# Optimization experiments

Hardware: AMD Instinct MI355X
Metric: run time of the kernel (lower is better)

Reference implementation:

```python
import jax, jax.numpy as jnp
import numpy as np

BLOCK_SIZE = 64
TOP_K = 4
D_MODEL = 256


def setup_inputs() -> dict:
    key = jax.random.key(0)
    kq, kk, kv = jax.random.split(key, 3)
    B, N, D = 4, 4096, D_MODEL
    q = jax.random.normal(kq, (B, N, D), dtype=jnp.float32)
    k = jax.random.normal(kk, (B, N, D), dtype=jnp.float32)
    v = jax.random.normal(kv, (B, N, D), dtype=jnp.float32)
    return {"q": q, "k": k, "v": v}


def _block_sparse_mask(q, k):
    # q, k: (B, N, D). Returns (B, N, N) bool mask (True = keep).
    B, N, D = q.shape
    nb = N // BLOCK_SIZE
    q_cent = q.reshape(B, nb, BLOCK_SIZE, D).mean(axis=2)  # (B, nb, D)
    k_cent = k.reshape(B, nb, BLOCK_SIZE, D).mean(axis=2)  # (B, nb, D)
    # pairwise Euclidean distance between centroids (nb is small: 64)
    diff = q_cent[:, :, None, :] - k_cent[:, None, :, :]   # (B, nb, nb, D)
    dist = jnp.sqrt(jnp.sum(diff * diff, axis=-1))          # (B, nb, nb)
    kk_ = min(TOP_K, nb)
    _, top_idx = jax.lax.top_k(-dist, kk_)                  # smallest distances
    mask = jnp.zeros((B, nb, nb), dtype=bool)
    b_idx = jnp.arange(B)[:, None, None]
    r_idx = jnp.arange(nb)[None, :, None]
    mask = mask.at[b_idx, r_idx, top_idx].set(True)
    # expand block mask to full (B, N, N) via broadcast-reshape
    mask_full = jnp.broadcast_to(
        mask[:, :, None, :, None], (B, nb, BLOCK_SIZE, nb, BLOCK_SIZE)
    ).reshape(B, N, N)
    return mask_full


def reference(q, k, v):
    mask = _block_sparse_mask(q, k)
    scale = 1.0 / (D_MODEL ** 0.5)
    scores = jnp.einsum('bqd,bkd->bqk', q, k) * scale       # (B, N, N)
    scores = jnp.where(mask, scores, -jnp.inf)
    attn = jax.nn.softmax(scores, axis=-1)
    out = jnp.einsum('bqk,bkd->bqd', attn, v)               # (B, N, D)
    return out
```

## Files before the change

kernel.cpp:

```cpp
#include <hip/hip_runtime.h>
#include <math.h>
#include <stdint.h>

#define BATCH 4
#define NSEQ 4096
#define DM 256
#define BLK 64
#define NB 64
#define TOPK 4

typedef unsigned short u16;
typedef unsigned int u32;
typedef __attribute__((ext_vector_type(8))) short bf16x8;
typedef __attribute__((ext_vector_type(4))) float f32x4;

__device__ __forceinline__ u16 f2bf(float f) {
    union { float f; u32 u; } c{f};
    u32 r = c.u + 0x7FFFu + ((c.u >> 16) & 1u);
    return (u16)(r >> 16);
}
__device__ __forceinline__ float bf2f(u16 h) {
    union { u32 u; float f; } c{((u32)h) << 16};
    return c.f;
}

__global__ __launch_bounds__(256) void prep_kernel(
    const float* __restrict__ q, const float* __restrict__ k, const float* __restrict__ v,
    u16* __restrict__ qh, u16* __restrict__ ql, u16* __restrict__ kh, u16* __restrict__ kl,
    u16* __restrict__ vtg, float* __restrict__ qc, float* __restrict__ kc)
{
    __shared__ u16 vt[256 * 66];
    const int gblk = blockIdx.x;
    const int d = threadIdx.x;
    const size_t base = (size_t)gblk * (BLK * DM);

    float s = 0.f;
#pragma unroll 8
    for (int r = 0; r < BLK; ++r) {
        float x = q[base + (size_t)r * DM + d];
        s += x;
        u16 h = f2bf(x);
        qh[base + (size_t)r * DM + d] = h;
        ql[base + (size_t)r * DM + d] = f2bf(x - bf2f(h));
    }
    qc[(size_t)gblk * DM + d] = s * (1.f / BLK);

    s = 0.f;
#pragma unroll 8
    for (int r = 0; r < BLK; ++r) {
        float x = k[base + (size_t)r * DM + d];
        s += x;
        u16 h = f2bf(x);
        kh[base + (size_t)r * DM + d] = h;
        kl[base + (size_t)r * DM + d] = f2bf(x - bf2f(h));
    }
    kc[(size_t)gblk * DM + d] = s * (1.f / BLK);

#pragma unroll 8
    for (int r = 0; r < BLK; ++r)
        vt[d * 66 + r] = f2bf(v[base + (size_t)r * DM + d]);
    __syncthreads();

    const int w = threadIdx.x >> 6, lane = threadIdx.x & 63;
    const int half = lane >> 5, c = lane & 31;
    const u32* vts = (const u32*)vt;
    u32* vo = (u32*)vtg + (base >> 1);
#pragma unroll
    for (int i = 0; i < 32; ++i) {
        int dr = w * 64 + i * 2 + half;
        vo[dr * 32 + c] = vts[dr * 33 + c];
    }
}

__global__ __launch_bounds__(256) void topk_kernel(const float* __restrict__ qc,
                                                   const float* __restrict__ kc,
                                                   int* __restrict__ top4)
{
    extern __shared__ float kcl[];
    float* red = kcl + 64 * 258;
    const int bid = blockIdx.x;
    const int swz = (bid & 7) * 32 + (bid >> 3);
    const int b = swz >> 6;
    const int t = threadIdx.x;

    const float* kcb = kc + (size_t)(b * NB) * DM;
#pragma unroll
    for (int it = 0; it < 64; ++it) {
        int li = t + it * 256;
        kcl[(li >> 8) * 258 + (li & 255)] = kcb[li];
    }
    __syncthreads();

    const int j = t & 63, dq = t >> 6;
    const float* qrow = qc + (size_t)swz * DM;
    float s = 0.f;
#pragma unroll 8
    for (int dd = 0; dd < 64; ++dd) {
        float diff = qrow[dq * 64 + dd] - kcl[j * 258 + dq * 64 + dd];
        s += diff * diff;
    }
    red[dq * 64 + j] = s;
    __syncthreads();

    if (t < 64) {
        float dist = sqrtf(red[t] + red[64 + t] + red[128 + t] + red[192 + t]);
        for (int sel = 0; sel < TOPK; ++sel) {
            float mv = dist;
            int mi = t;
#pragma unroll
            for (int off = 32; off >= 1; off >>= 1) {
                float ov = __shfl_xor(mv, off);
                int oi = __shfl_xor(mi, off);
                if (ov < mv || (ov == mv && oi < mi)) { mv = ov; mi = oi; }
            }
            if (t == 0) top4[swz * 4 + sel] = mi;
            if (t == mi) dist = 3.0e38f;
        }
    }
}

#define QH_O 0
#define QL_O 16896
#define KH_O 33792
#define KL_O 50688
#define VT_O 33792

__global__ __launch_bounds__(256, 1) void attn_kernel(
    const u16* __restrict__ qh, const u16* __restrict__ ql,
    const u16* __restrict__ kh, const u16* __restrict__ kl,
    const u16* __restrict__ vtg, const int* __restrict__ top4, float* __restrict__ out)
{
    extern __shared__ u16 smem[];
    const int bid = blockIdx.x;
    const int swz = (bid & 7) * 32 + (bid >> 3);
    const int b = swz >> 6, qb = swz & 63;
    const int tid = threadIdx.x;
    const int w = tid >> 6, lane = tid & 63;
    const int x = lane & 15, g = lane >> 4;

    auto stage64 = [&](int dsthw, const u16* __restrict__ src) {
#pragma unroll
        for (int it = 0; it < 8; ++it) {
            int li = tid + it * 256;
            int row = li >> 5, c8 = li & 31;
            *(uint4*)&smem[dsthw + row * 264 + c8 * 8] = *(const uint4*)&src[row * 256 + c8 * 8];
        }
    };
    auto stageVt = [&](const u16* __restrict__ src) {
#pragma unroll
        for (int it = 0; it < 8; ++it) {
            int li = tid + it * 256;
            int dr = li >> 3, c8 = li & 7;
            *(uint4*)&smem[VT_O + dr * 72 + c8 * 8] = *(const uint4*)&src[dr * 64 + c8 * 8];
        }
    };

    int sel[TOPK];
#pragma unroll
    for (int t = 0; t < TOPK; ++t) sel[t] = top4[swz * 4 + t];

    const size_t qbase = (size_t)swz * (BLK * DM);
    stage64(QH_O, qh + qbase);
    stage64(QL_O, ql + qbase);
    {
        size_t kb0 = (size_t)(b * NB + sel[0]) * (BLK * DM);
        stage64(KH_O, kh + kb0);
        stage64(KL_O, kl + kb0);
    }
    __syncthreads();

    bf16x8 bqh[8], bql[8];
    const int qrow = w * 16 + x;
#pragma unroll
    for (int dc = 0; dc < 8; ++dc) {
        bqh[dc] = *(const bf16x8*)&smem[QH_O + qrow * 264 + dc * 32 + g * 8];
        bql[dc] = *(const bf16x8*)&smem[QL_O + qrow * 264 + dc * 32 + g * 8];
    }

    f32x4 S[16];
#pragma unroll
    for (int t = 0; t < 16; ++t) S[t] = (f32x4){0.f, 0.f, 0.f, 0.f};

#pragma unroll
    for (int kb = 0; kb < TOPK; ++kb) {
#pragma unroll
        for (int jt = 0; jt < 4; ++jt) {
            f32x4 acc = S[kb * 4 + jt];
#pragma unroll
            for (int dc = 0; dc < 8; ++dc) {
                bf16x8 ah = *(const bf16x8*)&smem[KH_O + (jt * 16 + x) * 264 + dc * 32 + g * 8];
                bf16x8 al = *(const bf16x8*)&smem[KL_O + (jt * 16 + x) * 264 + dc * 32 + g * 8];
                acc = __builtin_amdgcn_mfma_f32_16x16x32_bf16(ah, bqh[dc], acc, 0, 0, 0);
                acc = __builtin_amdgcn_mfma_f32_16x16x32_bf16(ah, bql[dc], acc, 0, 0, 0);
                acc = __builtin_amdgcn_mfma_f32_16x16x32_bf16(al, bqh[dc], acc, 0, 0, 0);
            }
            S[kb * 4 + jt] = acc;
        }
        __syncthreads();
        if (kb < TOPK - 1) {
            size_t kbn = (size_t)(b * NB + sel[kb + 1]) * (BLK * DM);
            stage64(KH_O, kh + kbn);
            stage64(KL_O, kl + kbn);
            __syncthreads();
        }
    }

    float mx = -3.0e38f;
#pragma unroll
    for (int t = 0; t < 16; ++t)
#pragma unroll
        for (int r = 0; r < 4; ++r) { S[t][r] *= 0.0625f; mx = fmaxf(mx, S[t][r]); }
    mx = fmaxf(mx, __shfl_xor(mx, 16));
    mx = fmaxf(mx, __shfl_xor(mx, 32));
    float sum = 0.f;
#pragma unroll
    for (int t = 0; t < 16; ++t)
#pragma unroll
        for (int r = 0; r < 4; ++r) { float p = __expf(S[t][r] - mx); S[t][r] = p; sum += p; }
    sum += __shfl_xor(sum, 16);
    sum += __shfl_xor(sum, 32);
    const float inv = 1.f / sum;

    stageVt(vtg + (size_t)(b * NB + sel[0]) * (BLK * DM));
    u32* pw = (u32*)smem;
#pragma unroll
    for (int t = 0; t < 16; ++t)
#pragma unroll
        for (int rp = 0; rp < 2; ++rp) {
            u32 dw = (u32)f2bf(S[t][2 * rp] * inv) | ((u32)f2bf(S[t][2 * rp + 1] * inv) << 16);
            pw[qrow * 132 + t * 8 + g * 2 + rp] = dw;
        }
    __syncthreads();

    f32x4 O[16];
#pragma unroll
    for (int t = 0; t < 16; ++t) O[t] = (f32x4){0.f, 0.f, 0.f, 0.f};

#pragma unroll
    for (int kb = 0; kb < TOPK; ++kb) {
#pragma unroll
        for (int jc = 0; jc < 2; ++jc) {
            bf16x8 pa = *(const bf16x8*)&smem[qrow * 264 + kb * 64 + jc * 32 + g * 8];
#pragma unroll
            for (int dt = 0; dt < 16; ++dt) {
                bf16x8 bv = *(const bf16x8*)&smem[VT_O + (dt * 16 + x) * 72 + jc * 32 + g * 8];
                O[dt] = __builtin_amdgcn_mfma_f32_16x16x32_bf16(pa, bv, O[dt], 0, 0, 0);
            }
        }
        __syncthreads();
        if (kb < TOPK - 1) {
            stageVt(vtg + (size_t)(b * NB + sel[kb + 1]) * (BLK * DM));
            __syncthreads();
        }
    }

    float* ob = out + ((size_t)b * NSEQ + (size_t)qb * BLK) * DM;
#pragma unroll
    for (int dt = 0; dt < 16; ++dt)
#pragma unroll
        for (int r = 0; r < 4; ++r)
            ob[(size_t)(w * 16 + g * 4 + r) * DM + dt * 16 + x] = O[dt][r];
}

extern "C" void kernel_launch(void* const* d_in, const int* in_sizes, int n_in,
                              void* d_out, int out_size, void* d_ws, size_t ws_size,
                              hipStream_t stream) {
    const float* q = (const float*)d_in[0];
    const float* k = (const float*)d_in[1];
    const float* v = (const float*)d_in[2];
    float* out = (float*)d_out;

    const size_t nelem = (size_t)BATCH * NSEQ * DM;
    u16* qh = (u16*)d_ws;
    u16* ql = qh + nelem;
    u16* kh = ql + nelem;
    u16* kl = kh + nelem;
    u16* vtg = kl + nelem;
    float* qc = (float*)(vtg + nelem);
    float* kc = qc + (size_t)BATCH * NB * DM;
    int* top4 = (int*)(kc + (size_t)BATCH * NB * DM);

    prep_kernel<<<BATCH * NB, 256, 0, stream>>>(q, k, v, qh, ql, kh, kl, vtg, qc, kc);

    const int tk_lds = (64 * 258 + 256) * (int)sizeof(float);
    hipFuncSetAttribute((const void*)topk_kernel, hipFuncAttributeMaxDynamicSharedMemorySize, tk_lds);
    topk_kernel<<<BATCH * NB, 256, tk_lds, stream>>>(qc, kc, top4);

    const int at_lds = 67584 * 2;
    hipFuncSetAttribute((const void*)attn_kernel, hipFuncAttributeMaxDynamicSharedMemorySize, at_lds);
    attn_kernel<<<BATCH * NB, 256, at_lds, stream>>>(qh, ql, kh, kl, vtg, top4, out);
}
```

Baseline: 135.1 us.

## Replace split-bf16 QK with single fp16 MFMA and halve LDS footprint

Drops the hi/lo bf16 split of Q and K, which needed three MFMAs per chunk, and stores Q, K, V and P as fp16 so QK^T needs a single fp16 MFMA. This removes the extra workspace writes and reads and most of the QK MFMA work, and halves attention LDS so two blocks can fit per CU under launch bounds (256,2). The V^T tile switches from padded rows to an XOR swizzle to avoid bank conflicts. Scores lose precision (fp16 rounding of unit-normal inputs) and fp16 has narrower range, which could affect tolerance.

```diff
diff --git a/kernel.cpp b/kernel.cpp
--- a/kernel.cpp
+++ b/kernel.cpp
@@ -11,23 +11,19 @@
 
 typedef unsigned short u16;
 typedef unsigned int u32;
-typedef __attribute__((ext_vector_type(8))) short bf16x8;
+typedef __attribute__((ext_vector_type(8))) _Float16 f16x8;
 typedef __attribute__((ext_vector_type(4))) float f32x4;
 
-__device__ __forceinline__ u16 f2bf(float f) {
-    union { float f; u32 u; } c{f};
-    u32 r = c.u + 0x7FFFu + ((c.u >> 16) & 1u);
-    return (u16)(r >> 16);
-}
-__device__ __forceinline__ float bf2f(u16 h) {
-    union { u32 u; float f; } c{((u32)h) << 16};
-    return c.f;
+__device__ __forceinline__ u16 f2h(float f) {
+    union { _Float16 h; u16 u; } c;
+    c.h = (_Float16)f;
+    return c.u;
 }
 
 __global__ __launch_bounds__(256) void prep_kernel(
     const float* __restrict__ q, const float* __restrict__ k, const float* __restrict__ v,
-    u16* __restrict__ qh, u16* __restrict__ ql, u16* __restrict__ kh, u16* __restrict__ kl,
-    u16* __restrict__ vtg, float* __restrict__ qc, float* __restrict__ kc)
+    u16* __restrict__ qf, u16* __restrict__ kf, u16* __restrict__ vtg,
+    float* __restrict__ qc, float* __restrict__ kc)
 {
     __shared__ u16 vt[256 * 66];
     const int gblk = blockIdx.x;
@@ -39,9 +35,7 @@
     for (int r = 0; r < BLK; ++r) {
         float x = q[base + (size_t)r * DM + d];
         s += x;
-        u16 h = f2bf(x);
-        qh[base + (size_t)r * DM + d] = h;
-        ql[base + (size_t)r * DM + d] = f2bf(x - bf2f(h));
+        qf[base + (size_t)r * DM + d] = f2h(x);
     }
     qc[(size_t)gblk * DM + d] = s * (1.f / BLK);
 
@@ -50,15 +44,13 @@
     for (int r = 0; r < BLK; ++r) {
         float x = k[base + (size_t)r * DM + d];
         s += x;
-        u16 h = f2bf(x);
-        kh[base + (size_t)r * DM + d] = h;
-        kl[base + (size_t)r * DM + d] = f2bf(x - bf2f(h));
+        kf[base + (size_t)r * DM + d] = f2h(x);
     }
     kc[(size_t)gblk * DM + d] = s * (1.f / BLK);
 
 #pragma unroll 8
     for (int r = 0; r < BLK; ++r)
-        vt[d * 66 + r] = f2bf(v[base + (size_t)r * DM + d]);
+        vt[d * 66 + r] = f2h(v[base + (size_t)r * DM + d]);
     __syncthreads();
 
     const int w = threadIdx.x >> 6, lane = threadIdx.x & 63;
@@ -119,15 +111,11 @@
     }
 }
 
-#define QH_O 0
-#define QL_O 16896
-#define KH_O 33792
-#define KL_O 50688
-#define VT_O 33792
-
-__global__ __launch_bounds__(256, 1) void attn_kernel(
-    const u16* __restrict__ qh, const u16* __restrict__ ql,
-    const u16* __restrict__ kh, const u16* __restrict__ kl,
+#define KQ_O 16896
+#define VT_O 16896
+
+__global__ __launch_bounds__(256, 2) void attn_kernel(
+    const u16* __restrict__ qf, const u16* __restrict__ kf,
     const u16* __restrict__ vtg, const int* __restrict__ top4, float* __restrict__ out)
 {
     extern __shared__ u16 smem[];
@@ -151,7 +139,7 @@
         for (int it = 0; it < 8; ++it) {
             int li = tid + it * 256;
             int dr = li >> 3, c8 = li & 7;
-            *(uint4*)&smem[VT_O + dr * 72 + c8 * 8] = *(const uint4*)&src[dr * 64 + c8 * 8];
+            *(uint4*)&smem[VT_O + dr * 64 + (c8 ^ (dr & 7)) * 8] = *(const uint4*)&src[dr * 64 + c8 * 8];
         }
     };
 
@@ -160,22 +148,15 @@
     for (int t = 0; t < TOPK; ++t) sel[t] = top4[swz * 4 + t];
 
     const size_t qbase = (size_t)swz * (BLK * DM);
-    stage64(QH_O, qh + qbase);
-    stage64(QL_O, ql + qbase);
-    {
-        size_t kb0 = (size_t)(b * NB + sel[0]) * (BLK * DM);
-        stage64(KH_O, kh + kb0);
-        stage64(KL_O, kl + kb0);
-    }
-    __syncthreads();
-
-    bf16x8 bqh[8], bql[8];
+    stage64(0, qf + qbase);
+    stage64(KQ_O, kf + (size_t)(b * NB + sel[0]) * (BLK * DM));
+    __syncthreads();
+
+    f16x8 bq[8];
     const int qrow = w * 16 + x;
 #pragma unroll
-    for (int dc = 0; dc < 8; ++dc) {
-        bqh[dc] = *(const bf16x8*)&smem[QH_O + qrow * 264 + dc * 32 + g * 8];
-        bql[dc] = *(const bf16x8*)&smem[QL_O + qrow * 264 + dc * 32 + g * 8];
-    }
+    for (int dc = 0; dc < 8; ++dc)
+        bq[dc] = *(const f16x8*)&smem[qrow * 264 + dc * 32 + g * 8];
 
     f32x4 S[16];
 #pragma unroll
@@ -188,19 +169,14 @@
             f32x4 acc = S[kb * 4 + jt];
 #pragma unroll
             for (int dc = 0; dc < 8; ++dc) {
-                bf16x8 ah = *(const bf16x8*)&smem[KH_O + (jt * 16 + x) * 264 + dc * 32 + g * 8];
-                bf16x8 al = *(const bf16x8*)&smem[KL_O + (jt * 16 + x) * 264 + dc * 32 + g * 8];
-                acc = __builtin_amdgcn_mfma_f32_16x16x32_bf16(ah, bqh[dc], acc, 0, 0, 0);
-                acc = __builtin_amdgcn_mfma_f32_16x16x32_bf16(ah, bql[dc], acc, 0, 0, 0);
-                acc = __builtin_amdgcn_mfma_f32_16x16x32_bf16(al, bqh[dc], acc, 0, 0, 0);
+                f16x8 ak = *(const f16x8*)&smem[KQ_O + (jt * 16 + x) * 264 + dc * 32 + g * 8];
+                acc = __builtin_amdgcn_mfma_f32_16x16x32_f16(ak, bq[dc], acc, 0, 0, 0);
             }
             S[kb * 4 + jt] = acc;
         }
         __syncthreads();
         if (kb < TOPK - 1) {
-            size_t kbn = (size_t)(b * NB + sel[kb + 1]) * (BLK * DM);
-            stage64(KH_O, kh + kbn);
-            stage64(KL_O, kl + kbn);
+            stage64(KQ_O, kf + (size_t)(b * NB + sel[kb + 1]) * (BLK * DM));
             __syncthreads();
         }
     }
@@ -227,7 +203,7 @@
     for (int t = 0; t < 16; ++t)
 #pragma unroll
         for (int rp = 0; rp < 2; ++rp) {
-            u32 dw = (u32)f2bf(S[t][2 * rp] * inv) | ((u32)f2bf(S[t][2 * rp + 1] * inv) << 16);
+            u32 dw = (u32)f2h(S[t][2 * rp] * inv) | ((u32)f2h(S[t][2 * rp + 1] * inv) << 16);
             pw[qrow * 132 + t * 8 + g * 2 + rp] = dw;
         }
     __syncthreads();
@@ -240,11 +216,11 @@
     for (int kb = 0; kb < TOPK; ++kb) {
 #pragma unroll
         for (int jc = 0; jc < 2; ++jc) {
-            bf16x8 pa = *(const bf16x8*)&smem[qrow * 264 + kb * 64 + jc * 32 + g * 8];
+            f16x8 pa = *(const f16x8*)&smem[qrow * 264 + kb * 64 + jc * 32 + g * 8];
 #pragma unroll
             for (int dt = 0; dt < 16; ++dt) {
-                bf16x8 bv = *(const bf16x8*)&smem[VT_O + (dt * 16 + x) * 72 + jc * 32 + g * 8];
-                O[dt] = __builtin_amdgcn_mfma_f32_16x16x32_bf16(pa, bv, O[dt], 0, 0, 0);
+                f16x8 bv = *(const f16x8*)&smem[VT_O + (dt * 16 + x) * 64 + ((jc * 4 + g) ^ (x & 7)) * 8];
+                O[dt] = __builtin_amdgcn_mfma_f32_16x16x32_f16(pa, bv, O[dt], 0, 0, 0);
             }
         }
         __syncthreads();
@@ -271,22 +247,20 @@
     float* out = (float*)d_out;
 
     const size_t nelem = (size_t)BATCH * NSEQ * DM;
-    u16* qh = (u16*)d_ws;
-    u16* ql = qh + nelem;
-    u16* kh = ql + nelem;
-    u16* kl = kh + nelem;
-    u16* vtg = kl + nelem;
+    u16* qf = (u16*)d_ws;
+    u16* kf = qf + nelem;
+    u16* vtg = kf + nelem;
     float* qc = (float*)(vtg + nelem);
     float* kc = qc + (size_t)BATCH * NB * DM;
     int* top4 = (int*)(kc + (size_t)BATCH * NB * DM);
 
-    prep_kernel<<<BATCH * NB, 256, 0, stream>>>(q, k, v, qh, ql, kh, kl, vtg, qc, kc);
+    prep_kernel<<<BATCH * NB, 256, 0, stream>>>(q, k, v, qf, kf, vtg, qc, kc);
 
     const int tk_lds = (64 * 258 + 256) * (int)sizeof(float);
     hipFuncSetAttribute((const void*)topk_kernel, hipFuncAttributeMaxDynamicSharedMemorySize, tk_lds);
     topk_kernel<<<BATCH * NB, 256, tk_lds, stream>>>(qc, kc, top4);
 
-    const int at_lds = 67584 * 2;
+    const int at_lds = 33792 * 2;
     hipFuncSetAttribute((const void*)attn_kernel, hipFuncAttributeMaxDynamicSharedMemorySize, at_lds);
-    attn_kernel<<<BATCH * NB, 256, at_lds, stream>>>(qh, ql, kh, kl, vtg, top4, out);
-}
+    attn_kernel<<<BATCH * NB, 256, at_lds, stream>>>(qf, kf, vtg, top4, out);
+}
```

Measured after the change: 121.7 us. 1.11x faster.
